# Optimization experiments

Measured on AMD Instinct MI355X. Metric: run time of the kernel, lower is better.

The kernel has to match this reference:

```python
import jax, jax.numpy as jnp
import numpy as np

MIXTURE_COUNT = 4
GAUSSIANS_PER_MIXTURE = 4
EM_ITERS = 3
EPS = 1e-4


def setup_inputs() -> dict:
    key = jax.random.key(0)
    k1, k2 = jax.random.split(key)
    B, C, N = 1, 3, 1048576
    input_tensor = jax.random.normal(k1, (B, C, N), dtype=jnp.float32)
    label_tensor = jax.random.randint(k2, (B, N), 0, MIXTURE_COUNT, dtype=jnp.int32)
    return {"input_tensor": input_tensor, "label_tensor": label_tensor}


def _gmm_em(x, mix_oh, M, G):
    # x: [B,N,C] features, mix_oh: [B,N,M] one-hot mixture labels
    B, N, C = x.shape
    eye = jnp.eye(C, dtype=x.dtype)
    # init: split each mixture's pixels round-robin across its G gaussians
    sub_oh = jax.nn.one_hot(jnp.arange(N) % G, G, dtype=x.dtype)  # [N,G]
    resp = mix_oh[:, :, :, None] * sub_oh[None, :, None, :]       # [B,N,M,G]
    logp = None
    for _ in range(EM_ITERS):
        # ---- M-step: label-segmented weighted stats ----
        w = resp.sum(axis=1) + EPS                                 # [B,M,G]
        mu = jnp.einsum('bnmg,bnc->bmgc', resp, x) / w[..., None]  # [B,M,G,C]
        xx = jnp.einsum('bnmg,bnc,bnd->bmgcd', resp, x, x) / w[..., None, None]
        cov = xx - mu[..., :, None] * mu[..., None, :] + EPS * eye  # [B,M,G,C,C]
        prec = jnp.linalg.inv(cov)
        _, logdet = jnp.linalg.slogdet(cov)                        # [B,M,G]
        pi = w / w.sum(axis=2, keepdims=True)                      # [B,M,G]
        # ---- E-step: per-pixel Gaussian log-likelihoods ----
        # Mahalanobis via expansion to avoid [B,N,M,G,C] residual tensor
        xPx = jnp.einsum('bnc,bmgcd,bnd->bnmg', x, prec, x)
        xPm = jnp.einsum('bnc,bmgcd,bmgd->bnmg', x, prec, mu)
        mPm = jnp.einsum('bmgc,bmgcd,bmgd->bmg', mu, prec, mu)
        quad = xPx - 2.0 * xPm + mPm[:, None]                      # [B,N,M,G]
        logp = (jnp.log(pi)[:, None]
                - 0.5 * (quad + logdet[:, None] + C * jnp.log(2.0 * jnp.pi)))
        # pixels only redistribute among the gaussians of their own mixture
        resp = mix_oh[..., None] * jax.nn.softmax(logp, axis=3)
    return logp


def reference(input_tensor, label_tensor):
    M, G = MIXTURE_COUNT, GAUSSIANS_PER_MIXTURE
    x = jnp.swapaxes(input_tensor, 1, 2)                           # [B,N,C]
    mix_oh = jax.nn.one_hot(label_tensor, M, dtype=x.dtype)        # [B,N,M]
    logp = _gmm_em(x, mix_oh, M, G)                                # [B,N,M,G]
    # posterior over mixtures for every pixel
    mix_log = jax.nn.logsumexp(logp, axis=3)                       # [B,N,M]
    post = jax.nn.softmax(mix_log, axis=2)
    return jnp.swapaxes(post, 1, 2)                                # [B,M,N]
```

## Files before the change

kernel.cpp:

```cpp
#include <hip/hip_runtime.h>
#include <math.h>


#define NTHR  256
#define NBLK  1024
#define NBANK 8
#define EPS_F 1e-4f
#define LOG2PI3 5.5136311992280366f

template<int CTRL>
__device__ __forceinline__ float dpp_f(float v) {
    return __int_as_float(
        __builtin_amdgcn_mov_dpp(__float_as_int(v), CTRL, 0xF, 0xF, false));
}
template<int CTRL>
__device__ __forceinline__ int dpp_i(int v) {
    return __builtin_amdgcn_mov_dpp(v, CTRL, 0xF, 0xF, false);
}


static __device__ void compute_params(const float* __restrict__ sumsIn,
                                      float* spar, float* sums, float* wtab,
                                      int tid) {
    if (tid < 160) {
        float4 v0 = ((const float4*)sumsIn)[tid * 2];
        float4 v1 = ((const float4*)sumsIn)[tid * 2 + 1];
        sums[tid] = ((v0.x + v0.y) + (v0.z + v0.w))
                  + ((v1.x + v1.y) + (v1.z + v1.w));
    }
    __syncthreads();
    if (tid < 16) wtab[tid] = sums[tid * 10] + EPS_F;
    __syncthreads();
    if (tid < 16) {
        const int tt = tid;
        const float* S = &sums[tt * 10];
        const float w  = wtab[tt];
        const float iw = 1.0f / w;
        float mu0 = S[1] * iw, mu1 = S[2] * iw, mu2 = S[3] * iw;
        float c00 = S[4] * iw - mu0 * mu0 + EPS_F;
        float c01 = S[5] * iw - mu0 * mu1;
        float c02 = S[6] * iw - mu0 * mu2;
        float c11 = S[7] * iw - mu1 * mu1 + EPS_F;
        float c12 = S[8] * iw - mu1 * mu2;
        float c22 = S[9] * iw - mu2 * mu2 + EPS_F;
        float d00 = c11 * c22 - c12 * c12;
        float d01 = c02 * c12 - c01 * c22;
        float d02 = c01 * c12 - c02 * c11;
        float det = c00 * d00 + c01 * d01 + c02 * d02;
        float idet = 1.0f / det;
        float P00 = d00 * idet, P01 = d01 * idet, P02 = d02 * idet;
        float P11 = (c00 * c22 - c02 * c02) * idet;
        float P12 = (c01 * c02 - c00 * c12) * idet;
        float P22 = (c00 * c11 - c01 * c01) * idet;
        float logdet = logf(det);
        const int mb = tt & 12;
        float wsum = wtab[mb] + wtab[mb + 1] + wtab[mb + 2] + wtab[mb + 3];
        float logpi = logf(w) - logf(wsum);
        float pm0 = P00 * mu0 + P01 * mu1 + P02 * mu2;
        float pm1 = P01 * mu0 + P11 * mu1 + P12 * mu2;
        float pm2 = P02 * mu0 + P12 * mu1 + P22 * mu2;
        float mPm = mu0 * pm0 + mu1 * pm1 + mu2 * pm2;
        float c0 = logpi - 0.5f * (mPm + logdet + LOG2PI3);
        float* P = spar + tt * 12;
        P[0] = pm0; P[1] = pm1; P[2] = pm2; P[3] = c0;
        P[4] = -0.5f * P00; P[5] = -0.5f * P11; P[6] = -0.5f * P22;
        P[7] = -P01; P[8] = -P02; P[9] = -P12;
        P[10] = 0.f; P[11] = 0.f;
    }
    __syncthreads();
}

#define ACC10(APTR, S)                                                      \
    {   float* A = (APTR);                                                  \
        A[0] += (S);                                                        \
        A[1] = fmaf((S), ra, A[1]);                                         \
        A[2] = fmaf((S), rb, A[2]);                                         \
        A[3] = fmaf((S), rc, A[3]);                                         \
        A[4] = fmaf((S), aa, A[4]);                                         \
        A[5] = fmaf((S), ab, A[5]);                                         \
        A[6] = fmaf((S), ac, A[6]);                                         \
        A[7] = fmaf((S), bb, A[7]);                                         \
        A[8] = fmaf((S), bc, A[8]);                                         \
        A[9] = fmaf((S), cc, A[9]);                                         }

#define SRC_STEP(SRC_)                                                      \
    {   const float ra = dpp_f<(SRC_) * 0x55>(a);                           \
        const float rb = dpp_f<(SRC_) * 0x55>(b);                           \
        const float rc = dpp_f<(SRC_) * 0x55>(c);                           \
        const int   rm = dpp_i<(SRC_) * 0x55>(m);                           \
        const bool sel = (rm == q);                                         \
        const float aa = ra * ra, ab = ra * rb, ac = ra * rc;               \
        const float bb = rb * rb, bc = rb * rc, cc = rc * rc;               \
        if (MODE) {                                                         \
            const float rw0 = dpp_f<(SRC_) * 0x55>(ws0);                    \
            const float rw1 = dpp_f<(SRC_) * 0x55>(ws1);                    \
            const float rw2 = dpp_f<(SRC_) * 0x55>(ws2);                    \
            const float rw3 = dpp_f<(SRC_) * 0x55>(ws3);                    \
            { const float s = sel ? rw0 : 0.f; ACC10(&acc[0],  s) }         \
            { const float s = sel ? rw1 : 0.f; ACC10(&acc[10], s) }         \
            { const float s = sel ? rw2 : 0.f; ACC10(&acc[20], s) }         \
            { const float s = sel ? rw3 : 0.f; ACC10(&acc[30], s) }         \
        } else {                                                            \
                                     \
            const float s = sel ? 1.f : 0.f;                                \
            ACC10(&acc[j * 10], s)                                          \
        }                                                                   \
    }

template<int MODE>
__global__ __launch_bounds__(NTHR, 2) void k_accum(const float* __restrict__ x,
                                                   const int* __restrict__ lab,
                                                   const float* __restrict__ sumsIn,
                                                   float* __restrict__ sumsOut,
                                                   int N) {
    __shared__ __align__(16) float spar[192];
    __shared__ float sums[160];
    __shared__ float wtab[16];
    __shared__ float sred[NTHR / 64][160];
    const int tid  = threadIdx.x;
    const int wave = tid >> 6, lane = tid & 63;
    const int q    = lane & 3;
    if (MODE) compute_params(sumsIn, spar, sums, wtab, tid);

    float acc[40];
    #pragma unroll
    for (int k = 0; k < 40; ++k) acc[k] = 0.f;

    const int groups = N >> 2;
    const int stride = gridDim.x * NTHR;
    const int gid    = blockIdx.x * NTHR + tid;
    const int trips  = (groups + stride - 1) / stride;
    const float4* x0p = (const float4*)x;
    const float4* x1p = (const float4*)(x + N);
    const float4* x2p = (const float4*)(x + 2 * N);
    const int4*   lp  = (const int4*)lab;

    for (int tr = 0; tr < trips; ++tr) {
        const int i  = tr * stride + gid;
        const bool valid = i < groups;
        const int ii = valid ? i : 0;
        float4 va = x0p[ii], vb = x1p[ii], vc = x2p[ii];
        int4   m4 = lp[ii];
        float pa[4] = {va.x, va.y, va.z, va.w};
        float pb[4] = {vb.x, vb.y, vb.z, vb.w};
        float pc[4] = {vc.x, vc.y, vc.z, vc.w};
        int   pm[4] = {m4.x, m4.y, m4.z, m4.w};
        if (!valid) { pm[0] = pm[1] = pm[2] = pm[3] = -1; }

        #pragma unroll
        for (int j = 0; j < 4; ++j) {
            const float a = pa[j], b = pb[j], c = pc[j];
            const int   m = pm[j];
            float ws0 = 0.f, ws1 = 0.f, ws2 = 0.f, ws3 = 0.f;
            if (MODE) {
                const float* P0 = spar + (m & 3) * 48;
                float l[4];
                #pragma unroll
                for (int g = 0; g < 4; ++g) {
                    const float* P = P0 + g * 12;
                    float4 q0 = *(const float4*)(P);
                    float4 q1 = *(const float4*)(P + 4);
                    float2 q2 = *(const float2*)(P + 8);
                    l[g] = q0.w + q0.x * a + q0.y * b + q0.z * c
                         + q1.x * (a * a) + q1.y * (b * b) + q1.z * (c * c)
                         + q1.w * (a * b) + q2.x * (a * c) + q2.y * (b * c);
                }
                float mx = fmaxf(fmaxf(l[0], l[1]), fmaxf(l[2], l[3]));
                float e0 = __expf(l[0] - mx), e1 = __expf(l[1] - mx);
                float e2 = __expf(l[2] - mx), e3 = __expf(l[3] - mx);
                float rs = 1.0f / (e0 + e1 + e2 + e3);
                ws0 = e0 * rs; ws1 = e1 * rs; ws2 = e2 * rs; ws3 = e3 * rs;
            }
            SRC_STEP(0) SRC_STEP(1) SRC_STEP(2) SRC_STEP(3)
        }
    }

    #pragma unroll
    for (int k = 0; k < 40; ++k) {
        float v = acc[k];
        v += dpp_f<0x124>(v);
        v += dpp_f<0x128>(v);
        v += __shfl_xor(v, 16, 64);
        v += __shfl_xor(v, 32, 64);
        acc[k] = v;
    }
    if (lane < 4) {
        #pragma unroll
        for (int k = 0; k < 40; ++k) sred[wave][lane * 40 + k] = acc[k];
    }
    __syncthreads();
    if (tid < 160) {
        float s = sred[0][tid] + sred[1][tid] + sred[2][tid] + sred[3][tid];
        unsafeAtomicAdd(&sumsOut[tid * NBANK + (blockIdx.x & (NBANK - 1))], s);
    }
}

__global__ __launch_bounds__(NTHR, 2) void k_final(const float* __restrict__ x,
                                                   const float* __restrict__ sumsIn,
                                                   float* __restrict__ out,
                                                   int N) {
    __shared__ __align__(16) float spar[192];
    __shared__ float sums[160];
    __shared__ float wtab[16];
    compute_params(sumsIn, spar, sums, wtab, threadIdx.x);
    const int lane = threadIdx.x & 63;
    const int q    = lane & 3;
    float PR[40];
    #pragma unroll
    for (int g = 0; g < 4; ++g)
        #pragma unroll
        for (int k = 0; k < 10; ++k) PR[g * 10 + k] = spar[q * 48 + g * 12 + k];

    const int groups = N >> 2;
    const int stride = gridDim.x * NTHR;
    const int gid    = blockIdx.x * NTHR + threadIdx.x;
    const int trips  = (groups + stride - 1) / stride;
    const float4* x0p = (const float4*)x;
    const float4* x1p = (const float4*)(x + N);
    const float4* x2p = (const float4*)(x + 2 * N);

#define FIN_P(P_)                                                           \
    {   const float ra = dpp_f<(P_) * 0x55>(a);                             \
        const float rb = dpp_f<(P_) * 0x55>(b);                             \
        const float rc = dpp_f<(P_) * 0x55>(c);                             \
        const float aa = ra * ra, ab = ra * rb, ac = ra * rc;               \
        const float bb = rb * rb, bc = rb * rc, cc = rc * rc;               \
        float l[4];                                                         \
        _Pragma("unroll")                                                   \
        for (int g = 0; g < 4; ++g) {                                       \
            const float* P = &PR[g * 10];                                   \
            l[g] = P[3] + P[0] * ra + P[1] * rb + P[2] * rc                 \
                 + P[4] * aa + P[5] * bb + P[6] * cc                        \
                 + P[7] * ab + P[8] * ac + P[9] * bc;                       \
        }                                                                   \
        float mx = fmaxf(fmaxf(l[0], l[1]), fmaxf(l[2], l[3]));             \
        M[P_] = mx + __logf(__expf(l[0] - mx) + __expf(l[1] - mx)          \
                          + __expf(l[2] - mx) + __expf(l[3] - mx));         \
    }

#define TRS(K_, QQ_)                                                        \
    {   const float v = dpp_f<(QQ_) * 0x55>(M[K_]);                         \
        if (q == (K_)) W[QQ_] = v;                                          }

    for (int tr = 0; tr < trips; ++tr) {
        const int i  = tr * stride + gid;
        const bool valid = i < groups;
        const int ii = valid ? i : 0;
        float4 va = x0p[ii], vb = x1p[ii], vc = x2p[ii];
        float pa[4] = {va.x, va.y, va.z, va.w};
        float pb[4] = {vb.x, vb.y, vb.z, vb.w};
        float pc[4] = {vc.x, vc.y, vc.z, vc.w};
        float po[4][4];

        #pragma unroll
        for (int j = 0; j < 4; ++j) {
            const float a = pa[j], b = pb[j], c = pc[j];
            float M[4];
            FIN_P(0) FIN_P(1) FIN_P(2) FIN_P(3)
            float W[4] = {0.f, 0.f, 0.f, 0.f};
            TRS(0, 0) TRS(0, 1) TRS(0, 2) TRS(0, 3)
            TRS(1, 0) TRS(1, 1) TRS(1, 2) TRS(1, 3)
            TRS(2, 0) TRS(2, 1) TRS(2, 2) TRS(2, 3)
            TRS(3, 0) TRS(3, 1) TRS(3, 2) TRS(3, 3)
            float mmx = fmaxf(fmaxf(W[0], W[1]), fmaxf(W[2], W[3]));
            float e0 = __expf(W[0] - mmx), e1 = __expf(W[1] - mmx);
            float e2 = __expf(W[2] - mmx), e3 = __expf(W[3] - mmx);
            float rs = 1.0f / (e0 + e1 + e2 + e3);
            po[j][0] = e0 * rs; po[j][1] = e1 * rs;
            po[j][2] = e2 * rs; po[j][3] = e3 * rs;
        }
        if (valid) {
            #pragma unroll
            for (int m = 0; m < 4; ++m) {
                ((float4*)(out + (size_t)m * N))[i] =
                    make_float4(po[0][m], po[1][m], po[2][m], po[3][m]);
            }
        }
    }
}

extern "C" void kernel_launch(void* const* d_in, const int* in_sizes, int n_in,
                              void* d_out, int out_size, void* d_ws, size_t ws_size,
                              hipStream_t stream) {
    const float* x   = (const float*)d_in[0];
    const int*   lab = (const int*)d_in[1];
    float* out = (float*)d_out;
    const int N = in_sizes[1];

    float* sums = (float*)d_ws;
    hipMemsetAsync(sums, 0, 3 * 160 * NBANK * sizeof(float), stream);

    dim3 grid(NBLK), blk(NTHR);
    k_accum<0><<<grid, blk, 0, stream>>>(x, lab, sums, sums, N);
    k_accum<1><<<grid, blk, 0, stream>>>(x, lab, sums, sums + 1280, N);
    k_accum<1><<<grid, blk, 0, stream>>>(x, lab, sums + 1280, sums + 2560, N);
    k_final<<<grid, blk, 0, stream>>>(x, sums + 2560, out, N);
}
```

Baseline: 171.9 us.

## Fuse EM passes into one persistent kernel with software grid barriers

Replaces the four separate kernel launches (three accumulation passes and the final posterior pass) with a single persistent kernel of 512 blocks. Blocks are synchronised between phases by an atomic-counter grid barrier that uses explicit cache-bypassing loads and atomics. The aim is to remove per-launch overhead and the idle gaps between dependent kernels. It relies on all 512 blocks being co-resident, which is needed to avoid deadlock; the poll loop has a timeout that could silently break correctness. The grid size is also halved.

```diff
diff --git a/kernel.cpp b/kernel.cpp
--- a/kernel.cpp
+++ b/kernel.cpp
@@ -3,10 +3,55 @@
 
 
 #define NTHR  256
-#define NBLK  1024
+#define NBLK  512
 #define NBANK 8
 #define EPS_F 1e-4f
 #define LOG2PI3 5.5136311992280366f
+
+typedef __attribute__((ext_vector_type(4))) float f32x4;
+
+__device__ __forceinline__ void atomic_add_dev(float* p, float v) {
+    asm volatile("global_atomic_add_f32 %0, %1, off sc1"
+                 :: "v"(p), "v"(v) : "memory");
+}
+__device__ __forceinline__ float sum_banks_dev(const float* p) {
+    f32x4 u, v;
+    asm volatile(
+        "global_load_dwordx4 %0, %2, off sc0 sc1\n\t"
+        "global_load_dwordx4 %1, %2, off offset:16 sc0 sc1\n\t"
+        "s_waitcnt vmcnt(0)"
+        : "=&v"(u), "=&v"(v)
+        : "v"(p)
+        : "memory");
+    return ((u.x + u.y) + (u.z + u.w)) + ((v.x + v.y) + (v.z + v.w));
+}
+__device__ __forceinline__ unsigned atomic_inc_ret_dev(unsigned* p) {
+    unsigned r, one = 1u;
+    asm volatile("global_atomic_add %0, %1, %2, off sc0 sc1\n\t"
+                 "s_waitcnt vmcnt(0)"
+                 : "=v"(r) : "v"(p), "v"(one) : "memory");
+    return r;
+}
+__device__ __forceinline__ unsigned load_u32_dev(const unsigned* p) {
+    unsigned r;
+    asm volatile("global_load_dword %0, %1, off sc0 sc1\n\t"
+                 "s_waitcnt vmcnt(0)"
+                 : "=v"(r) : "v"(p) : "memory");
+    return r;
+}
+
+__device__ __forceinline__ void gbar(unsigned* cnt, unsigned target) {
+    __syncthreads();
+    if (threadIdx.x == 0) {
+        atomic_inc_ret_dev(cnt);
+        unsigned polls = 0;
+        while (load_u32_dev(cnt) < target) {
+            __builtin_amdgcn_s_sleep(2);
+            if (++polls > (1u << 22)) break;
+        }
+    }
+    __syncthreads();
+}
 
 template<int CTRL>
 __device__ __forceinline__ float dpp_f(float v) {
@@ -23,10 +68,7 @@
                                       float* spar, float* sums, float* wtab,
                                       int tid) {
     if (tid < 160) {
-        float4 v0 = ((const float4*)sumsIn)[tid * 2];
-        float4 v1 = ((const float4*)sumsIn)[tid * 2 + 1];
-        sums[tid] = ((v0.x + v0.y) + (v0.z + v0.w))
-                  + ((v1.x + v1.y) + (v1.z + v1.w));
+        sums[tid] = sum_banks_dev(sumsIn + tid * NBANK);
     }
     __syncthreads();
     if (tid < 16) wtab[tid] = sums[tid * 10] + EPS_F;
@@ -108,73 +150,55 @@
     }
 
 template<int MODE>
-__global__ __launch_bounds__(NTHR, 2) void k_accum(const float* __restrict__ x,
-                                                   const int* __restrict__ lab,
-                                                   const float* __restrict__ sumsIn,
-                                                   float* __restrict__ sumsOut,
-                                                   int N) {
-    __shared__ __align__(16) float spar[192];
-    __shared__ float sums[160];
-    __shared__ float wtab[16];
-    __shared__ float sred[NTHR / 64][160];
-    const int tid  = threadIdx.x;
-    const int wave = tid >> 6, lane = tid & 63;
-    const int q    = lane & 3;
-    if (MODE) compute_params(sumsIn, spar, sums, wtab, tid);
-
-    float acc[40];
+__device__ __forceinline__ void accum_pix(float a, float b, float c, int m,
+                                          int j, const float* spar,
+                                          float* acc, int q) {
+    float ws0 = 0.f, ws1 = 0.f, ws2 = 0.f, ws3 = 0.f;
+    if (MODE) {
+        const float* P0 = spar + (m & 3) * 48;
+        float l[4];
+        #pragma unroll
+        for (int g = 0; g < 4; ++g) {
+            const float* P = P0 + g * 12;
+            float4 q0 = *(const float4*)(P);
+            float4 q1 = *(const float4*)(P + 4);
+            float2 q2 = *(const float2*)(P + 8);
+            l[g] = q0.w + q0.x * a + q0.y * b + q0.z * c
+                 + q1.x * (a * a) + q1.y * (b * b) + q1.z * (c * c)
+                 + q1.w * (a * b) + q2.x * (a * c) + q2.y * (b * c);
+        }
+        float mx = fmaxf(fmaxf(l[0], l[1]), fmaxf(l[2], l[3]));
+        float e0 = __expf(l[0] - mx), e1 = __expf(l[1] - mx);
+        float e2 = __expf(l[2] - mx), e3 = __expf(l[3] - mx);
+        float rs = 1.0f / (e0 + e1 + e2 + e3);
+        ws0 = e0 * rs; ws1 = e1 * rs; ws2 = e2 * rs; ws3 = e3 * rs;
+    }
+    SRC_STEP(0) SRC_STEP(1) SRC_STEP(2) SRC_STEP(3)
+}
+
+template<int MODE>
+__device__ __forceinline__ void accum_phase(const float4* x0p,
+                                            const float4* x1p,
+                                            const float4* x2p,
+                                            const int4* lp,
+                                            int groups, int stride, int gid,
+                                            const float* spar, float* acc,
+                                            int q) {
     #pragma unroll
     for (int k = 0; k < 40; ++k) acc[k] = 0.f;
-
-    const int groups = N >> 2;
-    const int stride = gridDim.x * NTHR;
-    const int gid    = blockIdx.x * NTHR + tid;
-    const int trips  = (groups + stride - 1) / stride;
-    const float4* x0p = (const float4*)x;
-    const float4* x1p = (const float4*)(x + N);
-    const float4* x2p = (const float4*)(x + 2 * N);
-    const int4*   lp  = (const int4*)lab;
-
-    for (int tr = 0; tr < trips; ++tr) {
-        const int i  = tr * stride + gid;
-        const bool valid = i < groups;
-        const int ii = valid ? i : 0;
-        float4 va = x0p[ii], vb = x1p[ii], vc = x2p[ii];
-        int4   m4 = lp[ii];
-        float pa[4] = {va.x, va.y, va.z, va.w};
-        float pb[4] = {vb.x, vb.y, vb.z, vb.w};
-        float pc[4] = {vc.x, vc.y, vc.z, vc.w};
-        int   pm[4] = {m4.x, m4.y, m4.z, m4.w};
-        if (!valid) { pm[0] = pm[1] = pm[2] = pm[3] = -1; }
-
-        #pragma unroll
-        for (int j = 0; j < 4; ++j) {
-            const float a = pa[j], b = pb[j], c = pc[j];
-            const int   m = pm[j];
-            float ws0 = 0.f, ws1 = 0.f, ws2 = 0.f, ws3 = 0.f;
-            if (MODE) {
-                const float* P0 = spar + (m & 3) * 48;
-                float l[4];
-                #pragma unroll
-                for (int g = 0; g < 4; ++g) {
-                    const float* P = P0 + g * 12;
-                    float4 q0 = *(const float4*)(P);
-                    float4 q1 = *(const float4*)(P + 4);
-                    float2 q2 = *(const float2*)(P + 8);
-                    l[g] = q0.w + q0.x * a + q0.y * b + q0.z * c
-                         + q1.x * (a * a) + q1.y * (b * b) + q1.z * (c * c)
-                         + q1.w * (a * b) + q2.x * (a * c) + q2.y * (b * c);
-                }
-                float mx = fmaxf(fmaxf(l[0], l[1]), fmaxf(l[2], l[3]));
-                float e0 = __expf(l[0] - mx), e1 = __expf(l[1] - mx);
-                float e2 = __expf(l[2] - mx), e3 = __expf(l[3] - mx);
-                float rs = 1.0f / (e0 + e1 + e2 + e3);
-                ws0 = e0 * rs; ws1 = e1 * rs; ws2 = e2 * rs; ws3 = e3 * rs;
-            }
-            SRC_STEP(0) SRC_STEP(1) SRC_STEP(2) SRC_STEP(3)
-        }
-    }
-
+    for (int i = gid; i < groups; i += stride) {
+        float4 va = x0p[i], vb = x1p[i], vc = x2p[i];
+        int4   m4 = lp[i];
+        accum_pix<MODE>(va.x, vb.x, vc.x, m4.x, 0, spar, acc, q);
+        accum_pix<MODE>(va.y, vb.y, vc.y, m4.y, 1, spar, acc, q);
+        accum_pix<MODE>(va.z, vb.z, vc.z, m4.z, 2, spar, acc, q);
+        accum_pix<MODE>(va.w, vb.w, vc.w, m4.w, 3, spar, acc, q);
+    }
+}
+
+__device__ __forceinline__ void reduce_atomic(float* acc, float (*sred)[160],
+                                              float* __restrict__ sumsOut,
+                                              int tid, int wave, int lane) {
     #pragma unroll
     for (int k = 0; k < 40; ++k) {
         float v = acc[k];
@@ -191,35 +215,16 @@
     __syncthreads();
     if (tid < 160) {
         float s = sred[0][tid] + sred[1][tid] + sred[2][tid] + sred[3][tid];
-        unsafeAtomicAdd(&sumsOut[tid * NBANK + (blockIdx.x & (NBANK - 1))], s);
-    }
-}
-
-__global__ __launch_bounds__(NTHR, 2) void k_final(const float* __restrict__ x,
-                                                   const float* __restrict__ sumsIn,
-                                                   float* __restrict__ out,
-                                                   int N) {
-    __shared__ __align__(16) float spar[192];
-    __shared__ float sums[160];
-    __shared__ float wtab[16];
-    compute_params(sumsIn, spar, sums, wtab, threadIdx.x);
-    const int lane = threadIdx.x & 63;
-    const int q    = lane & 3;
-    float PR[40];
-    #pragma unroll
-    for (int g = 0; g < 4; ++g)
-        #pragma unroll
-        for (int k = 0; k < 10; ++k) PR[g * 10 + k] = spar[q * 48 + g * 12 + k];
-
-    const int groups = N >> 2;
-    const int stride = gridDim.x * NTHR;
-    const int gid    = blockIdx.x * NTHR + threadIdx.x;
-    const int trips  = (groups + stride - 1) / stride;
-    const float4* x0p = (const float4*)x;
-    const float4* x1p = (const float4*)(x + N);
-    const float4* x2p = (const float4*)(x + 2 * N);
-
-#define FIN_P(P_)                                                           \
+        atomic_add_dev(&sumsOut[tid * NBANK + (blockIdx.x & (NBANK - 1))], s);
+    }
+    asm volatile("s_waitcnt vmcnt(0)" ::: "memory");
+}
+
+__device__ __forceinline__ void final_quad(float a, float b, float c,
+                                           const float* PR, int q,
+                                           float* W) {
+    float M[4];
+    #define FIN_P(P_)                                                       \
     {   const float ra = dpp_f<(P_) * 0x55>(a);                             \
         const float rb = dpp_f<(P_) * 0x55>(b);                             \
         const float rc = dpp_f<(P_) * 0x55>(c);                             \
@@ -237,44 +242,77 @@
         M[P_] = mx + __logf(__expf(l[0] - mx) + __expf(l[1] - mx)          \
                           + __expf(l[2] - mx) + __expf(l[3] - mx));         \
     }
-
-#define TRS(K_, QQ_)                                                        \
+    FIN_P(0) FIN_P(1) FIN_P(2) FIN_P(3)
+    #undef FIN_P
+    W[0] = W[1] = W[2] = W[3] = 0.f;
+    #define TRS(K_, QQ_)                                                    \
     {   const float v = dpp_f<(QQ_) * 0x55>(M[K_]);                         \
         if (q == (K_)) W[QQ_] = v;                                          }
-
-    for (int tr = 0; tr < trips; ++tr) {
-        const int i  = tr * stride + gid;
-        const bool valid = i < groups;
-        const int ii = valid ? i : 0;
-        float4 va = x0p[ii], vb = x1p[ii], vc = x2p[ii];
-        float pa[4] = {va.x, va.y, va.z, va.w};
-        float pb[4] = {vb.x, vb.y, vb.z, vb.w};
-        float pc[4] = {vc.x, vc.y, vc.z, vc.w};
+    TRS(0, 0) TRS(0, 1) TRS(0, 2) TRS(0, 3)
+    TRS(1, 0) TRS(1, 1) TRS(1, 2) TRS(1, 3)
+    TRS(2, 0) TRS(2, 1) TRS(2, 2) TRS(2, 3)
+    TRS(3, 0) TRS(3, 1) TRS(3, 2) TRS(3, 3)
+    #undef TRS
+    float mmx = fmaxf(fmaxf(W[0], W[1]), fmaxf(W[2], W[3]));
+    float e0 = __expf(W[0] - mmx), e1 = __expf(W[1] - mmx);
+    float e2 = __expf(W[2] - mmx), e3 = __expf(W[3] - mmx);
+    float rs = 1.0f / (e0 + e1 + e2 + e3);
+    W[0] = e0 * rs; W[1] = e1 * rs; W[2] = e2 * rs; W[3] = e3 * rs;
+}
+
+__global__ __launch_bounds__(NTHR, 2) void k_fused(const float* __restrict__ x,
+                                                   const int* __restrict__ lab,
+                                                   float* __restrict__ sums,
+                                                   unsigned* __restrict__ bar,
+                                                   float* __restrict__ out,
+                                                   int N) {
+    __shared__ __align__(16) float spar[192];
+    __shared__ float sumsh[160];
+    __shared__ float wtab[16];
+    __shared__ float sred[NTHR / 64][160];
+    const int tid  = threadIdx.x;
+    const int wave = tid >> 6, lane = tid & 63;
+    const int q    = lane & 3;
+    const int groups = N >> 2;
+    const int stride = gridDim.x * NTHR;
+    const int gid    = blockIdx.x * NTHR + tid;
+    const float4* x0p = (const float4*)x;
+    const float4* x1p = (const float4*)(x + N);
+    const float4* x2p = (const float4*)(x + 2 * N);
+    const int4*   lp  = (const int4*)lab;
+
+    float acc[40];
+
+    accum_phase<0>(x0p, x1p, x2p, lp, groups, stride, gid, spar, acc, q);
+    reduce_atomic(acc, sred, sums, tid, wave, lane);
+    gbar(bar, NBLK);
+
+    #pragma unroll 1
+    for (int p = 0; p < 2; ++p) {
+        compute_params(sums + p * 1280, spar, sumsh, wtab, tid);
+        accum_phase<1>(x0p, x1p, x2p, lp, groups, stride, gid, spar, acc, q);
+        reduce_atomic(acc, sred, sums + (p + 1) * 1280, tid, wave, lane);
+        gbar(bar, NBLK * (2 + p));
+    }
+
+    compute_params(sums + 2560, spar, sumsh, wtab, tid);
+    float PR[40];
+    #pragma unroll
+    for (int g = 0; g < 4; ++g)
+        #pragma unroll
+        for (int k = 0; k < 10; ++k) PR[g * 10 + k] = spar[q * 48 + g * 12 + k];
+
+    for (int i = gid; i < groups; i += stride) {
+        float4 va = x0p[i], vb = x1p[i], vc = x2p[i];
         float po[4][4];
-
+        final_quad(va.x, vb.x, vc.x, PR, q, po[0]);
+        final_quad(va.y, vb.y, vc.y, PR, q, po[1]);
+        final_quad(va.z, vb.z, vc.z, PR, q, po[2]);
+        final_quad(va.w, vb.w, vc.w, PR, q, po[3]);
         #pragma unroll
-        for (int j = 0; j < 4; ++j) {
-            const float a = pa[j], b = pb[j], c = pc[j];
-            float M[4];
-            FIN_P(0) FIN_P(1) FIN_P(2) FIN_P(3)
-            float W[4] = {0.f, 0.f, 0.f, 0.f};
-            TRS(0, 0) TRS(0, 1) TRS(0, 2) TRS(0, 3)
-            TRS(1, 0) TRS(1, 1) TRS(1, 2) TRS(1, 3)
-            TRS(2, 0) TRS(2, 1) TRS(2, 2) TRS(2, 3)
-            TRS(3, 0) TRS(3, 1) TRS(3, 2) TRS(3, 3)
-            float mmx = fmaxf(fmaxf(W[0], W[1]), fmaxf(W[2], W[3]));
-            float e0 = __expf(W[0] - mmx), e1 = __expf(W[1] - mmx);
-            float e2 = __expf(W[2] - mmx), e3 = __expf(W[3] - mmx);
-            float rs = 1.0f / (e0 + e1 + e2 + e3);
-            po[j][0] = e0 * rs; po[j][1] = e1 * rs;
-            po[j][2] = e2 * rs; po[j][3] = e3 * rs;
-        }
-        if (valid) {
-            #pragma unroll
-            for (int m = 0; m < 4; ++m) {
-                ((float4*)(out + (size_t)m * N))[i] =
-                    make_float4(po[0][m], po[1][m], po[2][m], po[3][m]);
-            }
+        for (int m = 0; m < 4; ++m) {
+            ((float4*)(out + (size_t)m * N))[i] =
+                make_float4(po[0][m], po[1][m], po[2][m], po[3][m]);
         }
     }
 }
@@ -287,12 +325,9 @@
     float* out = (float*)d_out;
     const int N = in_sizes[1];
 
-    float* sums = (float*)d_ws;
-    hipMemsetAsync(sums, 0, 3 * 160 * NBANK * sizeof(float), stream);
-
-    dim3 grid(NBLK), blk(NTHR);
-    k_accum<0><<<grid, blk, 0, stream>>>(x, lab, sums, sums, N);
-    k_accum<1><<<grid, blk, 0, stream>>>(x, lab, sums, sums + 1280, N);
-    k_accum<1><<<grid, blk, 0, stream>>>(x, lab, sums + 1280, sums + 2560, N);
-    k_final<<<grid, blk, 0, stream>>>(x, sums + 2560, out, N);
-}
+    float* sums   = (float*)d_ws;
+    unsigned* bar = (unsigned*)(sums + 3 * 160 * NBANK);
+    hipMemsetAsync(d_ws, 0, (3 * 160 * NBANK + 4) * sizeof(float), stream);
+
+    k_fused<<<dim3(NBLK), dim3(NTHR), 0, stream>>>(x, lab, sums, bar, out, N);
+}
```

After: 159.8 us. 1.08x faster.
